# Performance work log

Hardware: AMD Instinct MI355X
Metric: run time of the kernel (lower is better)

## Reference

```python
import jax, jax.numpy as jnp
import numpy as np

BITS = 4
GROUP = 128
PACK = 32 // BITS  # 8 values per int32
MASK = (1 << BITS) - 1


def _unpack_weight(qweight, K, N):
    # qweight: [K//PACK, N] int32; PACK 4-bit values packed along K in each int32
    shifts = jnp.arange(PACK, dtype=jnp.int32) * BITS  # [PACK]
    w = (qweight[:, None, :] >> shifts[None, :, None]) & MASK  # [K//PACK, PACK, N]
    return w.reshape(K, N)


def _unpack_zeros(qzeros, G, N):
    # qzeros: [G, N//PACK] int32; PACK 4-bit values packed along N in each int32
    shifts = jnp.arange(PACK, dtype=jnp.int32) * BITS  # [PACK]
    z = (qzeros[:, :, None] >> shifts[None, None, :]) & MASK  # [G, N//PACK, PACK]
    return z.reshape(G, N)


def setup_inputs() -> dict:
    key = jax.random.key(0)
    k1, k2, k3, k4 = jax.random.split(key, 4)
    B, S, K, N = 4, 1024, 4096, 11008
    G = K // GROUP
    x = jax.random.normal(k1, (B, S, K), dtype=jnp.float32)
    qweight = jax.random.randint(k2, (K // PACK, N), 0, 2147483647, dtype=jnp.int32)
    qzeros = jax.random.randint(k3, (G, N // PACK), 0, 2147483647, dtype=jnp.int32)
    scales = jax.random.uniform(k4, (G, N), dtype=jnp.float32) * 0.01
    return {"x": x, "qweight": qweight, "qzeros": qzeros, "scales": scales}


def reference(x, qweight, qzeros, scales):
    K = x.shape[-1]
    G, N = scales.shape
    # dequantize: W[k, n] = (q[k, n] - zero[g(k), n]) * scale[g(k), n]
    w_q = _unpack_weight(qweight, K, N).astype(jnp.float32)   # [K, N]
    zeros = _unpack_zeros(qzeros, G, N).astype(jnp.float32)   # [G, N]
    gid = jnp.arange(K) // GROUP                              # [K]
    W = (w_q - zeros[gid]) * scales[gid]                      # [K, N]
    return jnp.einsum('bsk,kn->bsn', x, W)
```

## Files before the change

### kernel.cpp

```cpp
#include <hip/hip_runtime.h>


#define BK 32
#define LDK 40
#define TILE_BYTES 10240
#define WTILE_BYTES 20480

typedef _Float16 v8h __attribute__((ext_vector_type(8)));
typedef _Float16 half2v __attribute__((ext_vector_type(2)));
typedef float v4f __attribute__((ext_vector_type(4)));

__device__ __forceinline__ unsigned pkrtz_u32(float a, float b) {
  return __builtin_bit_cast(unsigned, __builtin_amdgcn_cvt_pkrtz(a, b));
}

__device__ __forceinline__ void load_lds_16B(const void* g, void* l) {
  __builtin_amdgcn_global_load_lds(
      (const __attribute__((address_space(1))) unsigned*)g,
      (__attribute__((address_space(3))) unsigned*)l, 16, 0, 0);
}

__global__ __launch_bounds__(320)
void prep_x(const float* __restrict__ x, unsigned short* __restrict__ xt, int K) {
  const int kt = blockIdx.x, mt = blockIdx.y;
  unsigned short* tile = xt + (size_t)(mt * (K / 32) + kt) * (TILE_BYTES / 2);
#pragma unroll
  for (int p = 0; p < 2; ++p) {
    const int c = threadIdx.x + p * 320;
    const int r = c / 5, j = c - r * 5;
    uint4 o = {0u, 0u, 0u, 0u};
    if (j < 4) {
      const float* src = x + (size_t)(mt * 128 + r) * K + kt * 32 + j * 8;
      const float4 v0 = ((const float4*)src)[0];
      const float4 v1 = ((const float4*)src)[1];
      o.x = pkrtz_u32(v0.x, v0.y); o.y = pkrtz_u32(v0.z, v0.w);
      o.z = pkrtz_u32(v1.x, v1.y); o.w = pkrtz_u32(v1.z, v1.w);
    }
    *(uint4*)((char*)tile + (size_t)c * 16) = o;
  }
}

__global__ __launch_bounds__(256)
void prep_w(const unsigned* __restrict__ qweight,
            const unsigned* __restrict__ qzeros,
            const float* __restrict__ scales,
            unsigned short* __restrict__ wt, int N, int K) {
  const int nt = blockIdx.x, kt = blockIdx.y;
  const int g = kt >> 2;
  unsigned short* tile = wt + (size_t)(nt * (K / 32) + kt) * (WTILE_BYTES / 2);
#pragma unroll
  for (int p = 0; p < 5; ++p) {
    const int c = threadIdx.x + p * 256;
    const int n = c / 5, j = c - n * 5;
    const int gn = nt * 256 + n;
    uint4 o = {0u, 0u, 0u, 0u};
    if (j < 4) {
      const unsigned zp = qzeros[(size_t)g * (N >> 3) + (gn >> 3)];
      const float s = scales[(size_t)g * N + gn];
      const unsigned z = (zp >> ((gn & 7) * 4)) & 15u;
      const unsigned hz_u = 0x64006400u | z | (z << 16);
      const half2v hz2 = __builtin_bit_cast(half2v, hz_u);
      const half2v hs2 = __builtin_bit_cast(half2v, pkrtz_u32(s, s));
      const unsigned qv = qweight[(size_t)(kt * 4 + j) * N + gn];
      unsigned* wp = (unsigned*)&o;
#pragma unroll
      for (int b = 0; b < 4; ++b) {
        const unsigned byte = qv >> (8 * b);
        const unsigned pq = 0x64006400u | (byte & 0xFu) | ((byte & 0xF0u) << 12);
        const half2v w2 = (__builtin_bit_cast(half2v, pq) - hz2) * hs2;
        wp[b] = __builtin_bit_cast(unsigned, w2);
      }
    }
    *(uint4*)((char*)tile + (size_t)c * 16) = o;
  }
}

__global__ __launch_bounds__(512, 4)
void qgemm_pre(const unsigned short* __restrict__ xt,
               const unsigned short* __restrict__ wt,
               float* __restrict__ out, int M, int N, int K) {
  __shared__ __align__(16) short As[2][128][LDK];
  __shared__ __align__(16) short Bs[2][256][LDK];

  const int tid = threadIdx.x;
  const int lane = tid & 63;
  const int wid = tid >> 6;

  const int gx = gridDim.x;
  const int nwg = gx * gridDim.y;
  int bid = blockIdx.x + gx * blockIdx.y;
  {
    const int xcd = bid & 7;
    const int idx = bid >> 3;
    const int q = nwg >> 3, r = nwg & 7;
    bid = (xcd < r ? xcd * (q + 1) : r * (q + 1) + (xcd - r) * q) + idx;
  }
  const int mt = bid % gx;
  const int nt = bid / gx;
  const int n0 = nt * 256, m0 = mt * 128;
  const int wm = (wid >> 2) * 64;
  const int wn = (wid & 3) * 64;
  const int lr = lane & 15;
  const int lk = (lane >> 4) * 8;

  const int NT = K / BK;
  const char* ga0 = (const char*)xt + (size_t)mt * NT * TILE_BYTES +
                    wid * 1024 + lane * 16;
  const char* gb0 = (const char*)wt + (size_t)nt * NT * WTILE_BYTES +
                    wid * 1024 + lane * 16;

  v4f acc[4][4] = {};

  auto stage = [&](int b, int t) {
    const char* ga = ga0 + (size_t)t * TILE_BYTES;
    const char* gb = gb0 + (size_t)t * WTILE_BYTES;
    char* la = ((char*)&As[b][0][0]) + wid * 1024;
    char* lb = ((char*)&Bs[b][0][0]) + wid * 1024;
    load_lds_16B(ga, la);
    if (wid < 2) load_lds_16B(ga + 8 * 1024, la + 8 * 1024);
    load_lds_16B(gb, lb);
    load_lds_16B(gb + 8 * 1024, lb + 8 * 1024);
    if (wid < 4) load_lds_16B(gb + 16 * 1024, lb + 16 * 1024);
  };

  auto compute = [&](int b) {
    v8h af[4], bfr[4];
#pragma unroll
    for (int i = 0; i < 4; ++i) {
      af[i] = *(const v8h*)(&As[b][wm + i * 16 + lr][lk]);
      bfr[i] = *(const v8h*)(&Bs[b][wn + i * 16 + lr][lk]);
    }
    __builtin_amdgcn_s_setprio(1);
#pragma unroll
    for (int mi = 0; mi < 4; ++mi) {
#pragma unroll
      for (int ni = 0; ni < 4; ++ni) {
        acc[mi][ni] = __builtin_amdgcn_mfma_f32_16x16x32_f16(
            af[mi], bfr[ni], acc[mi][ni], 0, 0, 0);
      }
    }
    __builtin_amdgcn_s_setprio(0);
  };

  stage(0, 0);
  __syncthreads();

#pragma unroll 2
  for (int t = 0; t < NT - 1; ++t) {
    const int b = t & 1;
    stage(b ^ 1, t + 1);
    compute(b);
    __syncthreads();
  }
  compute((NT - 1) & 1);

#pragma unroll
  for (int mi = 0; mi < 4; ++mi) {
#pragma unroll
    for (int ni = 0; ni < 4; ++ni) {
#pragma unroll
      for (int r = 0; r < 4; ++r) {
        const int row = m0 + wm + mi * 16 + (lane >> 4) * 4 + r;
        const int col = n0 + wn + ni * 16 + lr;
        out[(size_t)row * N + col] = acc[mi][ni][r];
      }
    }
  }
}

__global__ __launch_bounds__(512, 4)
void qgemm_dma(const unsigned short* __restrict__ xt,
               const unsigned* __restrict__ qweight,
               const unsigned* __restrict__ qzeros,
               const float* __restrict__ scales,
               float* __restrict__ out, int M, int N, int K) {
  __shared__ __align__(16) short As[128][LDK];
  __shared__ __align__(16) short Bs[256][LDK];

  const int tid = threadIdx.x;
  const int lane = tid & 63;
  const int wid = tid >> 6;
  const int n0 = blockIdx.x * 256;
  const int m0 = blockIdx.y * 128;
  const int mt = blockIdx.y;
  const int wm = (wid >> 2) * 64;
  const int wn = (wid & 3) * 64;
  const int lr = lane & 15;
  const int lk = (lane >> 4) * 8;

  const int b_n = tid & 255;
  const int b_kr0 = tid >> 8;
  const int gn = n0 + b_n;
  const unsigned* qwb = qweight + (size_t)b_kr0 * N + gn;

  const char* xt_b = (const char*)xt;
  const int NT = K / BK;

  v4f acc[4][4] = {};

  unsigned b0c, b1c, zpc;
  float scc;
  auto load_b = [&](int t, unsigned& b0, unsigned& b1, unsigned& zp, float& sc) {
    const int kk = t * BK;
    const size_t qoff = (size_t)(kk >> 3) * N;
    b0 = qwb[qoff];
    b1 = qwb[qoff + 2 * (size_t)N];
    const int g = kk >> 7;
    zp = qzeros[(size_t)g * (N >> 3) + (gn >> 3)];
    sc = scales[(size_t)g * N + gn];
  };
  load_b(0, b0c, b1c, zpc, scc);

#pragma unroll 2
  for (int t = 0; t < NT; ++t) {
    {
      const char* g = xt_b + (size_t)(mt * NT + t) * TILE_BYTES +
                      (size_t)wid * 1024 + (size_t)lane * 16;
      char* l = ((char*)&As[0][0]) + wid * 1024;
      load_lds_16B(g, l);
      if (wid < 2) load_lds_16B(g + 8 * 1024, l + 8 * 1024);
    }
    {
      const unsigned z = (zpc >> ((gn & 7) * 4)) & 15u;
      const unsigned hz_u = 0x64006400u | z | (z << 16);
      const half2v hz2 = __builtin_bit_cast(half2v, hz_u);
      const half2v hs2 = __builtin_bit_cast(half2v, pkrtz_u32(scc, scc));
      const unsigned qvs[2] = {b0c, b1c};
#pragma unroll
      for (int q = 0; q < 2; ++q) {
        const int kr = b_kr0 + q * 2;
        const unsigned qv = qvs[q];
        uint4 wv;
        unsigned* wp = (unsigned*)&wv;
#pragma unroll
        for (int j = 0; j < 4; ++j) {
          const unsigned byte = qv >> (8 * j);
          const unsigned pq = 0x64006400u | (byte & 0xFu) | ((byte & 0xF0u) << 12);
          const half2v w2 = (__builtin_bit_cast(half2v, pq) - hz2) * hs2;
          wp[j] = __builtin_bit_cast(unsigned, w2);
        }
        *(uint4*)(&Bs[b_n][kr * 8]) = wv;
      }
    }

    __syncthreads();

    unsigned b0n, b1n, zpn;
    float scn;
    const int tn = (t + 1 < NT) ? (t + 1) : t;
    load_b(tn, b0n, b1n, zpn, scn);

    v8h af[4], bfr[4];
#pragma unroll
    for (int i = 0; i < 4; ++i) {
      af[i] = *(const v8h*)(&As[wm + i * 16 + lr][lk]);
      bfr[i] = *(const v8h*)(&Bs[wn + i * 16 + lr][lk]);
    }
#pragma unroll
    for (int mi = 0; mi < 4; ++mi) {
#pragma unroll
      for (int ni = 0; ni < 4; ++ni) {
        acc[mi][ni] = __builtin_amdgcn_mfma_f32_16x16x32_f16(
            af[mi], bfr[ni], acc[mi][ni], 0, 0, 0);
      }
    }

    __syncthreads();

    b0c = b0n; b1c = b1n; zpc = zpn; scc = scn;
  }

#pragma unroll
  for (int mi = 0; mi < 4; ++mi) {
#pragma unroll
    for (int ni = 0; ni < 4; ++ni) {
#pragma unroll
      for (int r = 0; r < 4; ++r) {
        const int row = m0 + wm + mi * 16 + (lane >> 4) * 4 + r;
        const int col = n0 + wn + ni * 16 + lr;
        out[(size_t)row * N + col] = acc[mi][ni][r];
      }
    }
  }
}

__global__ __launch_bounds__(256, 2)
void qgemm_fused(const float* __restrict__ x,
                 const unsigned* __restrict__ qweight,
                 const unsigned* __restrict__ qzeros,
                 const float* __restrict__ scales,
                 float* __restrict__ out, int M, int N, int K) {
  __shared__ short As[128][LDK];
  __shared__ short Bs[128][LDK];

  const int tid = threadIdx.x;
  const int lane = tid & 63;
  const int wid = tid >> 6;
  const int n0 = blockIdx.x * 128;
  const int m0 = blockIdx.y * 128;
  const int wm = (wid >> 1) * 64;
  const int wn = (wid & 1) * 64;
  const int lr = lane & 15;
  const int lk = (lane >> 4) * 8;

  const int a_row = tid >> 3;
  const int a_col = (tid & 7) * 4;
  const int b_n = tid & 127;
  const int b_kr0 = tid >> 7;
  const int gn = n0 + b_n;

  const float* xb = x + (size_t)(m0 + a_row) * K + a_col;
  const unsigned* qwb = qweight + (size_t)b_kr0 * N + gn;

  v4f acc[4][4] = {};
  const int NT = K / BK;

  float4 axc[4];
  unsigned b0c, b1c, zpc;
  float scc;

  auto load_step = [&](int t, float4 ax[4], unsigned& b0, unsigned& b1,
                       unsigned& zp, float& sc) {
    const int kk = t * BK;
#pragma unroll
    for (int p = 0; p < 4; ++p)
      ax[p] = *(const float4*)(xb + (size_t)(p * 32) * K + kk);
    const size_t qoff = (size_t)(kk >> 3) * N;
    b0 = qwb[qoff];
    b1 = qwb[qoff + 2 * (size_t)N];
    const int g = kk >> 7;
    zp = qzeros[(size_t)g * (N >> 3) + (gn >> 3)];
    sc = scales[(size_t)g * N + gn];
  };

  load_step(0, axc, b0c, b1c, zpc, scc);

#pragma unroll 2
  for (int t = 0; t < NT; ++t) {
    const unsigned z = (zpc >> ((gn & 7) * 4)) & 15u;
    const unsigned hz_u = 0x64006400u | z | (z << 16);
    const half2v hz2 = __builtin_bit_cast(half2v, hz_u);
    const half2v hs2 = __builtin_bit_cast(half2v, pkrtz_u32(scc, scc));

#pragma unroll
    for (int p = 0; p < 4; ++p) {
      const int row = p * 32 + a_row;
      uint2 pv;
      pv.x = pkrtz_u32(axc[p].x, axc[p].y);
      pv.y = pkrtz_u32(axc[p].z, axc[p].w);
      *(uint2*)(&As[row][a_col]) = pv;
    }
    {
      const unsigned qvs[2] = {b0c, b1c};
#pragma unroll
      for (int q = 0; q < 2; ++q) {
        const int kr = b_kr0 + q * 2;
        const unsigned qv = qvs[q];
        uint4 wv;
        unsigned* wp = (unsigned*)&wv;
#pragma unroll
        for (int j = 0; j < 4; ++j) {
          const unsigned byte = qv >> (8 * j);
          const unsigned pq = 0x64006400u | (byte & 0xFu) | ((byte & 0xF0u) << 12);
          const half2v w2 = (__builtin_bit_cast(half2v, pq) - hz2) * hs2;
          wp[j] = __builtin_bit_cast(unsigned, w2);
        }
        *(uint4*)(&Bs[b_n][kr * 8]) = wv;
      }
    }

    __syncthreads();

    float4 axn[4];
    unsigned b0n, b1n, zpn;
    float scn;
    const int tn = (t + 1 < NT) ? (t + 1) : t;
    load_step(tn, axn, b0n, b1n, zpn, scn);

    v8h af[4], bfr[4];
#pragma unroll
    for (int i = 0; i < 4; ++i) {
      af[i] = *(const v8h*)(&As[wm + i * 16 + lr][lk]);
      bfr[i] = *(const v8h*)(&Bs[wn + i * 16 + lr][lk]);
    }
#pragma unroll
    for (int mi = 0; mi < 4; ++mi) {
#pragma unroll
      for (int ni = 0; ni < 4; ++ni) {
        acc[mi][ni] = __builtin_amdgcn_mfma_f32_16x16x32_f16(
            af[mi], bfr[ni], acc[mi][ni], 0, 0, 0);
      }
    }

    __syncthreads();

#pragma unroll
    for (int p = 0; p < 4; ++p) axc[p] = axn[p];
    b0c = b0n; b1c = b1n; zpc = zpn; scc = scn;
  }

#pragma unroll
  for (int mi = 0; mi < 4; ++mi) {
#pragma unroll
    for (int ni = 0; ni < 4; ++ni) {
#pragma unroll
      for (int r = 0; r < 4; ++r) {
        const int row = m0 + wm + mi * 16 + (lane >> 4) * 4 + r;
        const int col = n0 + wn + ni * 16 + lr;
        out[(size_t)row * N + col] = acc[mi][ni][r];
      }
    }
  }
}

extern "C" void kernel_launch(void* const* d_in, const int* in_sizes, int n_in,
                              void* d_out, int out_size, void* d_ws, size_t ws_size,
                              hipStream_t stream) {
  const float* x = (const float*)d_in[0];
  const unsigned* qweight = (const unsigned*)d_in[1];
  const unsigned* qzeros = (const unsigned*)d_in[2];
  const float* scales = (const float*)d_in[3];
  float* out = (float*)d_out;

  const int K = 4096;
  const int N = 11008;
  const int M = in_sizes[0] / K;

  const size_t A_BYTES = (size_t)(M / 128) * (K / 32) * TILE_BYTES;
  const size_t W_BYTES = (size_t)(N / 256) * (K / 32) * WTILE_BYTES;

  if (ws_size >= A_BYTES + W_BYTES) {
    unsigned short* xt = (unsigned short*)d_ws;
    unsigned short* wtp = (unsigned short*)((char*)d_ws + A_BYTES);
    prep_x<<<dim3(K / 32, M / 128), 320, 0, stream>>>(x, xt, K);
    prep_w<<<dim3(N / 256, K / 32), 256, 0, stream>>>(qweight, qzeros, scales, wtp, N, K);
    qgemm_pre<<<dim3(M / 128, N / 256), 512, 0, stream>>>(xt, wtp, out, M, N, K);
  } else if (ws_size >= A_BYTES) {
    unsigned short* xt = (unsigned short*)d_ws;
    prep_x<<<dim3(K / 32, M / 128), 320, 0, stream>>>(x, xt, K);
    qgemm_dma<<<dim3(N / 256, M / 128), 512, 0, stream>>>(xt, qweight, qzeros, scales,
                                                          out, M, N, K);
  } else {
    qgemm_fused<<<dim3(N / 128, M / 128), 256, 0, stream>>>(x, qweight, qzeros, scales,
                                                            out, M, N, K);
  }
}
```

Baseline: 684.7 us.

## Replace pre-dequant GEMM with 256x256 tile, BK=64 swizzled 8-wave pipelined kernel

Swaps the 128x256 tile, BK=32 padded-LDS GEMM for a 256x256 macro-tile kernel with BK=64. The new tiles are pre-laid-out in XOR-swizzled fp16 form by new prep kernels, so no LDS padding is needed. The main loop is hand-scheduled as quarter-tile MFMA blocks interleaved with global_load_lds prefetches, explicit s_barrier calls and vmcnt waits. The larger tile is meant to raise arithmetic intensity and reduce LDS bank conflicts, at the cost of more registers and LDS per block (occupancy bound drops to 2) and a new M%256 requirement.

```diff
diff --git a/kernel.cpp b/kernel.cpp
--- a/kernel.cpp
+++ b/kernel.cpp
@@ -4,7 +4,6 @@
 #define BK 32
 #define LDK 40
 #define TILE_BYTES 10240
-#define WTILE_BYTES 20480
 
 typedef _Float16 v8h __attribute__((ext_vector_type(8)));
 typedef _Float16 half2v __attribute__((ext_vector_type(2)));
@@ -18,6 +17,209 @@
   __builtin_amdgcn_global_load_lds(
       (const __attribute__((address_space(1))) unsigned*)g,
       (__attribute__((address_space(3))) unsigned*)l, 16, 0, 0);
+}
+
+__device__ __forceinline__ void bar() { asm volatile("s_barrier" ::: "memory"); }
+
+__global__ __launch_bounds__(512)
+void prep_a8(const float* __restrict__ x, unsigned short* __restrict__ fa, int K) {
+  const int t = blockIdx.x, mt = blockIdx.y;
+  unsigned short* tile = fa + (size_t)(mt * (K / 64) + t) * 16384;
+#pragma unroll
+  for (int p = 0; p < 4; ++p) {
+    const int c = threadIdx.x + p * 512;
+    const int h = c >> 10, r = (c >> 3) & 127, s = c & 7;
+    const float* src = x + (size_t)(mt * 256 + h * 128 + r) * K + t * 64 + s * 8;
+    const float4 v0 = ((const float4*)src)[0];
+    const float4 v1 = ((const float4*)src)[1];
+    uint4 o;
+    o.x = pkrtz_u32(v0.x, v0.y); o.y = pkrtz_u32(v0.z, v0.w);
+    o.z = pkrtz_u32(v1.x, v1.y); o.w = pkrtz_u32(v1.z, v1.w);
+    *(uint4*)(tile + h * 8192 + r * 64 + ((s ^ (r & 7)) << 3)) = o;
+  }
+}
+
+__global__ __launch_bounds__(512)
+void prep_b8(const unsigned* __restrict__ qweight,
+             const unsigned* __restrict__ qzeros,
+             const float* __restrict__ scales,
+             unsigned short* __restrict__ fb, int N, int K) {
+  const int nt = blockIdx.x, t = blockIdx.y;
+  const int g = t >> 1;
+  unsigned short* tile = fb + (size_t)(nt * (K / 64) + t) * 16384;
+#pragma unroll
+  for (int p = 0; p < 4; ++p) {
+    const int c = threadIdx.x + p * 512;
+    const int h = c >> 10, r = (c >> 3) & 127, s = c & 7;
+    const int n = nt * 256 + h * 128 + r;
+    const unsigned zp = qzeros[(size_t)g * (N >> 3) + (n >> 3)];
+    const float sc = scales[(size_t)g * N + n];
+    const unsigned z = (zp >> ((n & 7) * 4)) & 15u;
+    const unsigned hz_u = 0x64006400u | z | (z << 16);
+    const half2v hz2 = __builtin_bit_cast(half2v, hz_u);
+    const half2v hs2 = __builtin_bit_cast(half2v, pkrtz_u32(sc, sc));
+    const unsigned qv = qweight[(size_t)(t * 8 + s) * N + n];
+    uint4 o;
+    unsigned* wp = (unsigned*)&o;
+#pragma unroll
+    for (int b = 0; b < 4; ++b) {
+      const unsigned byte = qv >> (8 * b);
+      const unsigned pq = 0x64006400u | (byte & 0xFu) | ((byte & 0xF0u) << 12);
+      const half2v w2 = (__builtin_bit_cast(half2v, pq) - hz2) * hs2;
+      wp[b] = __builtin_bit_cast(unsigned, w2);
+    }
+    *(uint4*)(tile + h * 8192 + r * 64 + ((s ^ (r & 7)) << 3)) = o;
+  }
+}
+
+
+#define READA4(PA, MB)                                                         \
+  _Pragma("unroll") for (int i = 0; i < 4; ++i) {                              \
+    aF[i][0] = *(const v8h*)((PA) + ((MB + i) * 16 + lr16) * 128 + koff0);     \
+    aF[i][1] = *(const v8h*)((PA) + ((MB + i) * 16 + lr16) * 128 + koff1);     \
+  }
+
+#define READB2(PB, BF, NB)                                                     \
+  _Pragma("unroll") for (int j = 0; j < 2; ++j) {                              \
+    BF[j][0] = *(const v8h*)((PB) + ((NB + j) * 16 + lr16) * 128 + koff0);     \
+    BF[j][1] = *(const v8h*)((PB) + ((NB + j) * 16 + lr16) * 128 + koff1);     \
+  }
+
+#define MMAQ(MB, NB, BF)                                                       \
+  __builtin_amdgcn_s_setprio(1);                                              \
+  _Pragma("unroll") for (int i = 0; i < 4; ++i)                                \
+  _Pragma("unroll") for (int j = 0; j < 2; ++j) {                              \
+    acc[MB + i][NB + j] = __builtin_amdgcn_mfma_f32_16x16x32_f16(              \
+        aF[i][0], BF[j][0], acc[MB + i][NB + j], 0, 0, 0);                     \
+    acc[MB + i][NB + j] = __builtin_amdgcn_mfma_f32_16x16x32_f16(              \
+        aF[i][1], BF[j][1], acc[MB + i][NB + j], 0, 0, 0);                     \
+  }                                                                            \
+  __builtin_amdgcn_s_setprio(0);
+
+__global__ __launch_bounds__(512, 2)
+void qgemm8(const unsigned short* __restrict__ fa,
+            const unsigned short* __restrict__ fb,
+            float* __restrict__ out, int M, int N, int K) {
+  __shared__ __align__(16) short As[2][2][128][64];
+  __shared__ __align__(16) short Bs[2][2][128][64];
+
+  const int tid = threadIdx.x;
+  const int lane = tid & 63;
+  const int wid = tid >> 6;
+  const int wr = wid >> 2, wc = wid & 3;
+  const int lr16 = lane & 15, hi4 = lane >> 4, l7 = lane & 7;
+  const int koff0 = ((hi4 ^ l7) << 4);
+  const int koff1 = (((4 + hi4) ^ l7) << 4);
+
+  const int nmt = M / 256;
+  const int nwg = nmt * (N / 256);
+  int bid = blockIdx.x;
+  {
+    const int xcd = bid & 7, idx = bid >> 3;
+    const int q = nwg >> 3, r = nwg & 7;
+    bid = (xcd < r ? xcd * (q + 1) : r * (q + 1) + (xcd - r) * q) + idx;
+  }
+  const int mt = bid % nmt;
+  const int nt = bid / nmt;
+
+  const int NT = K / 64;
+  const int NI = NT / 2;
+
+  const char* srcA = (const char*)fa + (size_t)mt * NT * 32768 + wid * 1024 + lane * 16;
+  const char* srcB = (const char*)fb + (size_t)nt * NT * 32768 + wid * 1024 + lane * 16;
+  char* ldsA = (char*)&As[0][0][0][0];
+  char* ldsB = (char*)&Bs[0][0][0][0];
+  char* dstA = ldsA + wid * 1024;
+  char* dstB = ldsB + wid * 1024;
+
+  auto stageA = [&](int T, int h) {
+    const char* s = srcA + (size_t)T * 32768 + h * 16384;
+    char* d = dstA + (T & 1) * 32768 + h * 16384;
+    load_lds_16B(s, d);
+    load_lds_16B(s + 8192, d + 8192);
+  };
+  auto stageB = [&](int T, int h) {
+    const char* s = srcB + (size_t)T * 32768 + h * 16384;
+    char* d = dstB + (T & 1) * 32768 + h * 16384;
+    load_lds_16B(s, d);
+    load_lds_16B(s + 8192, d + 8192);
+  };
+
+  const char* pA[2] = {ldsA + wr * 16384, ldsA + 32768 + wr * 16384};
+  const char* pB[2] = {ldsB + (wc >> 1) * 16384 + (wc & 1) * 8192,
+                       ldsB + 32768 + (wc >> 1) * 16384 + (wc & 1) * 8192};
+
+  v4f acc[8][4] = {};
+  v8h aF[4][2], bL[2][2], bH[2][2];
+
+  stageB(0, 0); stageB(0, 1); stageA(0, 0); stageA(0, 1);
+  stageB(1, 0); stageB(1, 1);
+  asm volatile("s_waitcnt vmcnt(4)");
+  bar();
+
+  for (int it = 0; it < NI; ++it) {
+    const int t0 = 2 * it, t1 = 2 * it + 1;
+    const bool pf = (it < NI - 1);
+
+    READA4(pA[0], 0);
+    READB2(pA[0] == nullptr ? pB[0] : pB[0], bL, 0);
+    stageA(t1, 0);
+    bar();
+    MMAQ(0, 0, bL);
+    bar();
+    READB2(pB[0], bH, 2);
+    stageA(t1, 1);
+    bar();
+    MMAQ(0, 2, bH);
+    bar();
+    READA4(pA[0], 4);
+    if (pf) stageB(t0 + 2, 0);
+    bar();
+    MMAQ(4, 0, bL);
+    bar();
+    if (pf) { stageB(t0 + 2, 1); asm volatile("s_waitcnt vmcnt(4)"); }
+    else    { asm volatile("s_waitcnt vmcnt(0)"); }
+    bar();
+    MMAQ(4, 2, bH);
+    bar();
+
+    READA4(pA[1], 0);
+    READB2(pB[1], bL, 0);
+    if (pf) stageA(t0 + 2, 0);
+    bar();
+    MMAQ(0, 0, bL);
+    bar();
+    READB2(pB[1], bH, 2);
+    if (pf) stageA(t0 + 2, 1);
+    bar();
+    MMAQ(0, 2, bH);
+    bar();
+    READA4(pA[1], 4);
+    if (pf) stageB(t1 + 2, 0);
+    bar();
+    MMAQ(4, 0, bL);
+    bar();
+    if (pf) { stageB(t1 + 2, 1); asm volatile("s_waitcnt vmcnt(4)"); }
+    else    { asm volatile("s_waitcnt vmcnt(0)"); }
+    bar();
+    MMAQ(4, 2, bH);
+    bar();
+  }
+
+  const int m0 = mt * 256 + wr * 128;
+  const int n0 = nt * 256 + wc * 64;
+#pragma unroll
+  for (int mi = 0; mi < 8; ++mi) {
+#pragma unroll
+    for (int ni = 0; ni < 4; ++ni) {
+#pragma unroll
+      for (int r = 0; r < 4; ++r) {
+        const int row = m0 + mi * 16 + hi4 * 4 + r;
+        const int col = n0 + ni * 16 + lr16;
+        out[(size_t)row * N + col] = acc[mi][ni][r];
+      }
+    }
+  }
 }
 
 __global__ __launch_bounds__(320)
@@ -37,134 +239,6 @@
       o.z = pkrtz_u32(v1.x, v1.y); o.w = pkrtz_u32(v1.z, v1.w);
     }
     *(uint4*)((char*)tile + (size_t)c * 16) = o;
-  }
-}
-
-__global__ __launch_bounds__(256)
-void prep_w(const unsigned* __restrict__ qweight,
-            const unsigned* __restrict__ qzeros,
-            const float* __restrict__ scales,
-            unsigned short* __restrict__ wt, int N, int K) {
-  const int nt = blockIdx.x, kt = blockIdx.y;
-  const int g = kt >> 2;
-  unsigned short* tile = wt + (size_t)(nt * (K / 32) + kt) * (WTILE_BYTES / 2);
-#pragma unroll
-  for (int p = 0; p < 5; ++p) {
-    const int c = threadIdx.x + p * 256;
-    const int n = c / 5, j = c - n * 5;
-    const int gn = nt * 256 + n;
-    uint4 o = {0u, 0u, 0u, 0u};
-    if (j < 4) {
-      const unsigned zp = qzeros[(size_t)g * (N >> 3) + (gn >> 3)];
-      const float s = scales[(size_t)g * N + gn];
-      const unsigned z = (zp >> ((gn & 7) * 4)) & 15u;
-      const unsigned hz_u = 0x64006400u | z | (z << 16);
-      const half2v hz2 = __builtin_bit_cast(half2v, hz_u);
-      const half2v hs2 = __builtin_bit_cast(half2v, pkrtz_u32(s, s));
-      const unsigned qv = qweight[(size_t)(kt * 4 + j) * N + gn];
-      unsigned* wp = (unsigned*)&o;
-#pragma unroll
-      for (int b = 0; b < 4; ++b) {
-        const unsigned byte = qv >> (8 * b);
-        const unsigned pq = 0x64006400u | (byte & 0xFu) | ((byte & 0xF0u) << 12);
-        const half2v w2 = (__builtin_bit_cast(half2v, pq) - hz2) * hs2;
-        wp[b] = __builtin_bit_cast(unsigned, w2);
-      }
-    }
-    *(uint4*)((char*)tile + (size_t)c * 16) = o;
-  }
-}
-
-__global__ __launch_bounds__(512, 4)
-void qgemm_pre(const unsigned short* __restrict__ xt,
-               const unsigned short* __restrict__ wt,
-               float* __restrict__ out, int M, int N, int K) {
-  __shared__ __align__(16) short As[2][128][LDK];
-  __shared__ __align__(16) short Bs[2][256][LDK];
-
-  const int tid = threadIdx.x;
-  const int lane = tid & 63;
-  const int wid = tid >> 6;
-
-  const int gx = gridDim.x;
-  const int nwg = gx * gridDim.y;
-  int bid = blockIdx.x + gx * blockIdx.y;
-  {
-    const int xcd = bid & 7;
-    const int idx = bid >> 3;
-    const int q = nwg >> 3, r = nwg & 7;
-    bid = (xcd < r ? xcd * (q + 1) : r * (q + 1) + (xcd - r) * q) + idx;
-  }
-  const int mt = bid % gx;
-  const int nt = bid / gx;
-  const int n0 = nt * 256, m0 = mt * 128;
-  const int wm = (wid >> 2) * 64;
-  const int wn = (wid & 3) * 64;
-  const int lr = lane & 15;
-  const int lk = (lane >> 4) * 8;
-
-  const int NT = K / BK;
-  const char* ga0 = (const char*)xt + (size_t)mt * NT * TILE_BYTES +
-                    wid * 1024 + lane * 16;
-  const char* gb0 = (const char*)wt + (size_t)nt * NT * WTILE_BYTES +
-                    wid * 1024 + lane * 16;
-
-  v4f acc[4][4] = {};
-
-  auto stage = [&](int b, int t) {
-    const char* ga = ga0 + (size_t)t * TILE_BYTES;
-    const char* gb = gb0 + (size_t)t * WTILE_BYTES;
-    char* la = ((char*)&As[b][0][0]) + wid * 1024;
-    char* lb = ((char*)&Bs[b][0][0]) + wid * 1024;
-    load_lds_16B(ga, la);
-    if (wid < 2) load_lds_16B(ga + 8 * 1024, la + 8 * 1024);
-    load_lds_16B(gb, lb);
-    load_lds_16B(gb + 8 * 1024, lb + 8 * 1024);
-    if (wid < 4) load_lds_16B(gb + 16 * 1024, lb + 16 * 1024);
-  };
-
-  auto compute = [&](int b) {
-    v8h af[4], bfr[4];
-#pragma unroll
-    for (int i = 0; i < 4; ++i) {
-      af[i] = *(const v8h*)(&As[b][wm + i * 16 + lr][lk]);
-      bfr[i] = *(const v8h*)(&Bs[b][wn + i * 16 + lr][lk]);
-    }
-    __builtin_amdgcn_s_setprio(1);
-#pragma unroll
-    for (int mi = 0; mi < 4; ++mi) {
-#pragma unroll
-      for (int ni = 0; ni < 4; ++ni) {
-        acc[mi][ni] = __builtin_amdgcn_mfma_f32_16x16x32_f16(
-            af[mi], bfr[ni], acc[mi][ni], 0, 0, 0);
-      }
-    }
-    __builtin_amdgcn_s_setprio(0);
-  };
-
-  stage(0, 0);
-  __syncthreads();
-
-#pragma unroll 2
-  for (int t = 0; t < NT - 1; ++t) {
-    const int b = t & 1;
-    stage(b ^ 1, t + 1);
-    compute(b);
-    __syncthreads();
-  }
-  compute((NT - 1) & 1);
-
-#pragma unroll
-  for (int mi = 0; mi < 4; ++mi) {
-#pragma unroll
-    for (int ni = 0; ni < 4; ++ni) {
-#pragma unroll
-      for (int r = 0; r < 4; ++r) {
-        const int row = m0 + wm + mi * 16 + (lane >> 4) * 4 + r;
-        const int col = n0 + wn + ni * 16 + lr;
-        out[(size_t)row * N + col] = acc[mi][ni][r];
-      }
-    }
   }
 }
 
@@ -426,15 +500,16 @@
   const int N = 11008;
   const int M = in_sizes[0] / K;
 
+  const size_t A8 = (size_t)(M / 256) * (K / 64) * 32768;
+  const size_t B8 = (size_t)(N / 256) * (K / 64) * 32768;
   const size_t A_BYTES = (size_t)(M / 128) * (K / 32) * TILE_BYTES;
-  const size_t W_BYTES = (size_t)(N / 256) * (K / 32) * WTILE_BYTES;
-
-  if (ws_size >= A_BYTES + W_BYTES) {
-    unsigned short* xt = (unsigned short*)d_ws;
-    unsigned short* wtp = (unsigned short*)((char*)d_ws + A_BYTES);
-    prep_x<<<dim3(K / 32, M / 128), 320, 0, stream>>>(x, xt, K);
-    prep_w<<<dim3(N / 256, K / 32), 256, 0, stream>>>(qweight, qzeros, scales, wtp, N, K);
-    qgemm_pre<<<dim3(M / 128, N / 256), 512, 0, stream>>>(xt, wtp, out, M, N, K);
+
+  if ((M % 256 == 0) && ws_size >= A8 + B8) {
+    unsigned short* fa = (unsigned short*)d_ws;
+    unsigned short* fb = (unsigned short*)((char*)d_ws + A8);
+    prep_a8<<<dim3(K / 64, M / 256), 512, 0, stream>>>(x, fa, K);
+    prep_b8<<<dim3(N / 256, K / 64), 512, 0, stream>>>(qweight, qzeros, scales, fb, N, K);
+    qgemm8<<<dim3((M / 256) * (N / 256)), 512, 0, stream>>>(fa, fb, out, M, N, K);
   } else if (ws_size >= A_BYTES) {
     unsigned short* xt = (unsigned short*)d_ws;
     prep_x<<<dim3(K / 32, M / 128), 320, 0, stream>>>(x, xt, K);
```

Measured after the change: 622.1 us. 1.1x faster.
